# Kernel optimization log

Measured on AMD Instinct MI355X. Metric: run time of the kernel, lower is better.

## Reference

```python
import jax, jax.numpy as jnp
import numpy as np

N, E, D_IN, D_HID, D_OUT = 50000, 800000, 128, 128, 64

def setup_inputs() -> dict:
    key = jax.random.key(0)
    ks = jax.random.split(key, 20)
    inp = {
        'x': jax.random.normal(ks[0], (N, D_IN), dtype=jnp.float32),
        'edge_index': jax.random.randint(ks[1], (2, E), 0, N, dtype=jnp.int64),
        'edge_attr': jax.random.normal(ks[2], (E, 16), dtype=jnp.float32),
        'edge_weight': jax.random.uniform(ks[3], (E,), dtype=jnp.float32),
    }
    dims = [(D_IN, D_HID), (D_HID, D_HID), (D_HID, D_OUT)]
    for i, (di, do) in enumerate(dims):
        s = 1.0 / np.sqrt(di)
        inp[f'Wl{i}'] = jax.random.uniform(ks[4 + 5 * i], (di, do), minval=-s, maxval=s, dtype=jnp.float32)
        inp[f'bl{i}'] = jnp.zeros((do,), dtype=jnp.float32)
        inp[f'Wr{i}'] = jax.random.uniform(ks[5 + 5 * i], (di, do), minval=-s, maxval=s, dtype=jnp.float32)
        inp[f'Ws{i}'] = jax.random.uniform(ks[6 + 5 * i], (di, do), minval=-s, maxval=s, dtype=jnp.float32)
        inp[f'bs{i}'] = jnp.zeros((do,), dtype=jnp.float32)
    return inp


def _sage(x, src, dst, Wl, bl, Wr):
    # mean aggregation of source features at target nodes (PyG SAGEConv)
    msg = x[src]                                               # [E, d] gather
    ssum = jax.ops.segment_sum(msg, dst, num_segments=N)        # [N, d]
    cnt = jax.ops.segment_sum(jnp.ones((src.shape[0],), x.dtype), dst, num_segments=N)
    agg = ssum / jnp.maximum(cnt, 1.0)[:, None]
    return agg @ Wl + bl + x @ Wr                               # lin_l(agg) + lin_r(x)


def reference(x, edge_index, edge_attr, edge_weight,
              Wl0, bl0, Wr0, Ws0, bs0,
              Wl1, bl1, Wr1, Ws1, bs1,
              Wl2, bl2, Wr2, Ws2, bs2):
    src, dst = edge_index[0], edge_index[1]
    h = jax.nn.relu(_sage(x, src, dst, Wl0, bl0, Wr0) + x @ Ws0 + bs0)
    h = jax.nn.relu(_sage(h, src, dst, Wl1, bl1, Wr1) + h @ Ws1 + bs1)
    out = _sage(h, src, dst, Wl2, bl2, Wr2) + h @ Ws2 + bs2
    return out
```

## Files before the change

### kernel.cpp

```cpp
#include <hip/hip_runtime.h>
#include <hip/hip_bf16.h>


#define LB __launch_bounds__

typedef __attribute__((ext_vector_type(8))) short short8;
typedef __attribute__((ext_vector_type(4))) float f32x4;

__device__ __forceinline__ unsigned short bf16_rne(float f) {
  unsigned u = __builtin_bit_cast(unsigned, f);
  unsigned r = u + 0x7fffu + ((u >> 16) & 1u);
  return (unsigned short)(r >> 16);
}
__device__ __forceinline__ float bf16_to_f(unsigned short us) {
  return __builtin_bit_cast(float, (unsigned)us << 16);
}
__device__ __forceinline__ float bits_to_f(unsigned u) {
  return __builtin_bit_cast(float, u);
}

__device__ __forceinline__ void async16(const void* g, void* l) {
  __builtin_amdgcn_global_load_lds((const __attribute__((address_space(1))) unsigned*)g,
                                   (__attribute__((address_space(3))) unsigned*)l, 16, 0, 0);
}

#define BCAP 8192
#define P1_CHUNK 4096

__device__ __forceinline__ void p1_body(int bid, const int* __restrict__ src,
                                        const int* __restrict__ dst, int* __restrict__ bcnt,
                                        int2* __restrict__ pairs, int E) {
  __shared__ int cnt[256];
  __shared__ int base[256];
  const int tid = threadIdx.x;
  cnt[tid] = 0;
  __syncthreads();
  const int e0 = bid * P1_CHUNK;
  int myb[16], myr[16], mys[16], myd[16];
#pragma unroll
  for (int i = 0; i < 16; ++i) {
    int e = e0 + i * 256 + tid;
    myb[i] = -1;
    if (e < E) {
      int s = src[e], d = dst[e];
      int b = d >> 8;
      myb[i] = b;
      mys[i] = s;
      myd[i] = d;
      myr[i] = atomicAdd(&cnt[b], 1);
    }
  }
  __syncthreads();
  base[tid] = (cnt[tid] > 0) ? atomicAdd(&bcnt[tid], cnt[tid]) : 0;
  __syncthreads();
#pragma unroll
  for (int i = 0; i < 16; ++i) {
    int b = myb[i];
    if (b >= 0) {
      int p = base[b] + myr[i];
      if (p < BCAP) pairs[(size_t)b * BCAP + p] = make_int2(mys[i], myd[i]);
    }
  }
}

__device__ __forceinline__ void p234_body(int b, const int2* __restrict__ pairs,
                                          const int* __restrict__ bcnt, int* __restrict__ gcounter,
                                          int* __restrict__ row_start, int* __restrict__ deg_arr,
                                          float* __restrict__ scale, int* __restrict__ srcs, int N) {
  __shared__ int h[256];
  __shared__ int sc[256];
  __shared__ int cur[256];
  __shared__ int shared_bb;
  const int tid = threadIdx.x;
  h[tid] = 0;
  __syncthreads();
  int m = bcnt[b];
  if (m > BCAP) m = BCAP;
  for (int i = tid; i < m; i += 256) {
    atomicAdd(&h[pairs[(size_t)b * BCAP + i].y & 255], 1);
  }
  __syncthreads();
  const int deg = h[tid];
  sc[tid] = deg;
  __syncthreads();
  for (int off = 1; off < 256; off <<= 1) {
    int add = (tid >= off) ? sc[tid - off] : 0;
    __syncthreads();
    sc[tid] += add;
    __syncthreads();
  }
  if (tid == 0) shared_bb = atomicAdd(gcounter, sc[255]);
  __syncthreads();
  const int abs_off = shared_bb + sc[tid] - deg;
  const int node = b * 256 + tid;
  if (node < N) {
    row_start[node] = abs_off;
    deg_arr[node] = deg;
    scale[node] = 1.0f / (float)(deg > 1 ? deg : 1);
  }
  cur[tid] = abs_off;
  __syncthreads();
  for (int i = tid; i < m; i += 256) {
    int2 pr = pairs[(size_t)b * BCAP + i];
    int p = atomicAdd(&cur[pr.y & 255], 1);
    srcs[p] = pr.x;
  }
}

__device__ __forceinline__ void wpack_body(int wb, const float* __restrict__ Wl0,
                                           const float* __restrict__ Wr0,
                                           const float* __restrict__ Ws0,
                                           const float* __restrict__ bl0,
                                           const float* __restrict__ bs0,
                                           const float* __restrict__ Wl1,
                                           const float* __restrict__ Wr1,
                                           const float* __restrict__ Ws1,
                                           const float* __restrict__ bl1,
                                           const float* __restrict__ bs1,
                                           const float* __restrict__ Wl2,
                                           const float* __restrict__ Wr2,
                                           const float* __restrict__ Ws2,
                                           const float* __restrict__ bl2,
                                           const float* __restrict__ bs2, ushort* __restrict__ Bh0,
                                           ushort* __restrict__ Bo0, float* __restrict__ bb0,
                                           ushort* __restrict__ Bh1, ushort* __restrict__ Bo1,
                                           float* __restrict__ bb1, ushort* __restrict__ Bh2,
                                           ushort* __restrict__ Bo2, float* __restrict__ bb2) {
  const int layer = wb >> 7;
  const int xb = wb & 127;
  const float *Wl, *Wr, *Ws, *bl, *bs;
  ushort *Bh, *Bo;
  float* bb;
  int M;
  if (layer == 0) {
    Wl = Wl0; Wr = Wr0; Ws = Ws0; bl = bl0; bs = bs0; Bh = Bh0; Bo = Bo0; bb = bb0; M = 256;
  } else if (layer == 1) {
    Wl = Wl1; Wr = Wr1; Ws = Ws1; bl = bl1; bs = bs1; Bh = Bh1; Bo = Bo1; bb = bb1; M = 256;
  } else {
    Wl = Wl2; Wr = Wr2; Ws = Ws2; bl = bl2; bs = bs2; Bh = Bh2; Bo = Bo2; bb = bb2; M = 128;
  }
  const int DO = M / 2;
  int idx = xb * 256 + (int)threadIdx.x;
  if (idx < 128 * M) {
    int k = idx / M, c = idx - k * M;
    float v = (c < DO) ? Wl[k * DO + c] : (Wr[k * DO + (c - DO)] + Ws[k * DO + (c - DO)]);
    unsigned short h = bf16_rne(v);
    unsigned short l = bf16_rne(v - bf16_to_f(h));
    int d = ((k >> 3) * M + c) * 8 + (k & 7);
    Bh[d] = h;
    Bo[d] = l;
  }
  if (idx < DO) bb[idx] = bl[idx] + bs[idx];
}

__device__ __forceinline__ void split8v(f32x4 f0, f32x4 f1, short8& h, short8& l) {
  float f[8] = {f0[0], f0[1], f0[2], f0[3], f1[0], f1[1], f1[2], f1[3]};
#pragma unroll
  for (int j = 0; j < 8; ++j) {
    unsigned u = __builtin_bit_cast(unsigned, f[j]);
    h[j] = (short)(u >> 16);
    l[j] = (short)bf16_rne(f[j] - bits_to_f(u & 0xffff0000u));
  }
}

template <int M>
__device__ __forceinline__ void gemm_compute(int bx, const char* smem,
                                             const ushort* __restrict__ Bhi,
                                             const ushort* __restrict__ Blo,
                                             ushort* __restrict__ Yb, float* __restrict__ Z,
                                             int n) {
  constexpr int DO = M / 2;
  constexpr int NWC = (M >= 256) ? 4 : 2;
  constexpr int NWR = 4 / NWC;
  constexpr int BROWS = 32 * NWR;
  const int tid = threadIdx.x;
  const int w = tid >> 6, l = tid & 63;
  const int q = l >> 4, m16 = l & 15;
  const int rowBase = bx * BROWS + (w / NWC) * 32;
  const int colBase = (w % NWC) * 64;

  f32x4 acc[2][4] = {};
  const int rl0 = (w / NWC) * 32 + m16;

#pragma unroll
  for (int s = 0; s < 4; ++s) {
    short8 ah[2], al[2], bh[4], bo[4];
    const int kb = s * 4 + q;
#pragma unroll
    for (int i = 0; i < 2; ++i) {
      int rl = rl0 + i * 16;
      int g0 = (2 * kb) ^ m16;
      int g1 = (2 * kb + 1) ^ m16;
      f32x4 fa = *(const f32x4*)(smem + (size_t)rl * 512 + g0 * 16);
      f32x4 fb = *(const f32x4*)(smem + (size_t)rl * 512 + g1 * 16);
      split8v(fa, fb, ah[i], al[i]);
    }
#pragma unroll
    for (int j = 0; j < 4; ++j) {
      size_t off = ((size_t)kb * M + colBase + j * 16 + m16) * 8;
      bh[j] = *(const short8*)(Bhi + off);
      bo[j] = *(const short8*)(Blo + off);
    }
#pragma unroll
    for (int i = 0; i < 2; ++i)
#pragma unroll
      for (int j = 0; j < 4; ++j) {
        acc[i][j] = __builtin_amdgcn_mfma_f32_16x16x32_bf16(ah[i], bh[j], acc[i][j], 0, 0, 0);
        acc[i][j] = __builtin_amdgcn_mfma_f32_16x16x32_bf16(ah[i], bo[j], acc[i][j], 0, 0, 0);
        acc[i][j] = __builtin_amdgcn_mfma_f32_16x16x32_bf16(al[i], bh[j], acc[i][j], 0, 0, 0);
      }
  }

#pragma unroll
  for (int i = 0; i < 2; ++i) {
    int rb = rowBase + i * 16 + q * 4;
#pragma unroll
    for (int j = 0; j < 4; ++j) {
      int c = colBase + j * 16 + m16;
#pragma unroll
      for (int r = 0; r < 4; ++r) {
        int row = rb + r;
        if (row < n) {
          float v = acc[i][j][r];
          if (c < DO)
            Yb[(size_t)row * DO + c] = bf16_rne(v);
          else
            Z[(size_t)row * DO + (c - DO)] = v;
        }
      }
    }
  }
}

__device__ __forceinline__ void gemm0_body(int bx, const float* __restrict__ x,
                                           const ushort* __restrict__ Bh,
                                           const ushort* __restrict__ Bo, ushort* __restrict__ Yb,
                                           float* __restrict__ Z, int n, char* smem) {
  const int tid = threadIdx.x;
  const int wbase = tid & ~63;
#pragma unroll
  for (int r = 0; r < 4; ++r) {
    int ell = r * 256 + tid;
    int row = ell >> 5, gl = ell & 31;
    int grow = bx * 32 + row;
    if (grow >= n) grow = n - 1;
    int gs = gl ^ (row & 15);
    async16(x + (size_t)grow * 128 + gs * 4, smem + (size_t)(r * 256 + wbase) * 16);
  }
  __syncthreads();
  gemm_compute<256>(bx, smem, Bh, Bo, Yb, Z, n);
}

__device__ __forceinline__ void agg_gather128(const uint2* __restrict__ Yu,
                                              const int* __restrict__ srcs, int e0, int cnt,
                                              int lane, int li, int half, float& a0, float& a1,
                                              float& a2, float& a3) {
  const int end = e0 + cnt;
  const int c1 = cnt < 64 ? cnt : 64;
  int idx = (lane < c1) ? srcs[e0 + lane] : 0;
  int j = 0;
  for (; j + 16 <= c1; j += 16) {
    int s[8];
#pragma unroll
    for (int t = 0; t < 8; ++t) s[t] = __shfl(idx, j + 2 * t + half);
    uint2 u[8];
#pragma unroll
    for (int t = 0; t < 8; ++t) u[t] = Yu[(size_t)s[t] * 32 + li];
#pragma unroll
    for (int t = 0; t < 8; ++t) {
      a0 += bits_to_f(u[t].x << 16);
      a1 += bits_to_f(u[t].x & 0xffff0000u);
      a2 += bits_to_f(u[t].y << 16);
      a3 += bits_to_f(u[t].y & 0xffff0000u);
    }
  }
  if (j + 8 <= c1) {
    int s[4];
#pragma unroll
    for (int t = 0; t < 4; ++t) s[t] = __shfl(idx, j + 2 * t + half);
    uint2 u[4];
#pragma unroll
    for (int t = 0; t < 4; ++t) u[t] = Yu[(size_t)s[t] * 32 + li];
#pragma unroll
    for (int t = 0; t < 4; ++t) {
      a0 += bits_to_f(u[t].x << 16);
      a1 += bits_to_f(u[t].x & 0xffff0000u);
      a2 += bits_to_f(u[t].y << 16);
      a3 += bits_to_f(u[t].y & 0xffff0000u);
    }
    j += 8;
  }
  for (; j + 2 <= c1; j += 2) {
    int s = __shfl(idx, j + half);
    uint2 u = Yu[(size_t)s * 32 + li];
    a0 += bits_to_f(u.x << 16);
    a1 += bits_to_f(u.x & 0xffff0000u);
    a2 += bits_to_f(u.y << 16);
    a3 += bits_to_f(u.y & 0xffff0000u);
  }
  if (j < c1) {
    int s = __shfl(idx, j);
    if (half == 0) {
      uint2 u = Yu[(size_t)s * 32 + li];
      a0 += bits_to_f(u.x << 16);
      a1 += bits_to_f(u.x & 0xffff0000u);
      a2 += bits_to_f(u.y << 16);
      a3 += bits_to_f(u.y & 0xffff0000u);
    }
  }
  if (cnt > 64) {
    int e = e0 + 64;
    for (; e + 2 <= end; e += 2) {
      int s = srcs[e + half];
      uint2 u = Yu[(size_t)s * 32 + li];
      a0 += bits_to_f(u.x << 16);
      a1 += bits_to_f(u.x & 0xffff0000u);
      a2 += bits_to_f(u.y << 16);
      a3 += bits_to_f(u.y & 0xffff0000u);
    }
    if (e < end && half == 0) {
      int s = srcs[e];
      uint2 u = Yu[(size_t)s * 32 + li];
      a0 += bits_to_f(u.x << 16);
      a1 += bits_to_f(u.x & 0xffff0000u);
      a2 += bits_to_f(u.y << 16);
      a3 += bits_to_f(u.y & 0xffff0000u);
    }
  }
}

template <int M>
__global__ LB(256, 3) void fused_agg_gemm(const ushort* __restrict__ Y,
                                          const float* __restrict__ Zprev,
                                          const int* __restrict__ row_start,
                                          const int* __restrict__ deg_arr,
                                          const int* __restrict__ srcs,
                                          const float* __restrict__ scale,
                                          const float* __restrict__ bsum,
                                          const ushort* __restrict__ Bhi,
                                          const ushort* __restrict__ Blo, ushort* __restrict__ Yb,
                                          float* __restrict__ Zf, int n) {
  constexpr int BROWS = (M >= 256) ? 32 : 64;
  __shared__ __align__(16) char smem[BROWS * 512];
  const int tid = threadIdx.x;
  const int w = tid >> 6;
  const int lane = tid & 63;
  const int li = lane & 31;
  const int half = lane >> 5;
  const int blockRow0 = blockIdx.x * BROWS;
  const uint2* Yu = (const uint2*)Y;

#pragma unroll 1
  for (int t = 0; t < BROWS / 4; ++t) {
    const int r = t * 4 + w;
    const int node = blockRow0 + r;
    float a0 = 0.f, a1 = 0.f, a2 = 0.f, a3 = 0.f;
    const bool live = node < n;
    if (live) {
      agg_gather128(Yu, srcs, row_start[node], deg_arr[node], lane, li, half, a0, a1, a2, a3);
    }
    a0 += __shfl(a0, lane ^ 32);
    a1 += __shfl(a1, lane ^ 32);
    a2 += __shfl(a2, lane ^ 32);
    a3 += __shfl(a3, lane ^ 32);
    float4 o = make_float4(0.f, 0.f, 0.f, 0.f);
    if (live) {
      float sc = scale[node];
      float4 z = ((const float4*)Zprev)[(size_t)node * 32 + li];
      float4 b = ((const float4*)bsum)[li];
      o.x = fmaxf(z.x + sc * a0 + b.x, 0.f);
      o.y = fmaxf(z.y + sc * a1 + b.y, 0.f);
      o.z = fmaxf(z.z + sc * a2 + b.z, 0.f);
      o.w = fmaxf(z.w + sc * a3 + b.w, 0.f);
    }
    if (half == 0) {
      *(float4*)(smem + (size_t)r * 512 + (size_t)((li ^ (r & 15)) * 16)) = o;
    }
  }
  __syncthreads();
  gemm_compute<M>(blockIdx.x, smem, Bhi, Blo, Yb, Zf, n);
}

__global__ LB(256) void fused_wpack_p1(const int* __restrict__ src, const int* __restrict__ dst,
                                       int* __restrict__ bcnt, int2* __restrict__ pairs, int E,
                                       int NP1, const float* Wl0, const float* Wr0, const float* Ws0,
                                       const float* bl0, const float* bs0, const float* Wl1,
                                       const float* Wr1, const float* Ws1, const float* bl1,
                                       const float* bs1, const float* Wl2, const float* Wr2,
                                       const float* Ws2, const float* bl2, const float* bs2,
                                       ushort* Bh0, ushort* Bo0, float* bb0, ushort* Bh1,
                                       ushort* Bo1, float* bb1, ushort* Bh2, ushort* Bo2,
                                       float* bb2) {
  if ((int)blockIdx.x < NP1) {
    p1_body(blockIdx.x, src, dst, bcnt, pairs, E);
  } else {
    wpack_body(blockIdx.x - NP1, Wl0, Wr0, Ws0, bl0, bs0, Wl1, Wr1, Ws1, bl1, bs1, Wl2, Wr2, Ws2,
               bl2, bs2, Bh0, Bo0, bb0, Bh1, Bo1, bb1, Bh2, Bo2, bb2);
  }
}

__global__ LB(256, 3) void fused_p234_gemm0(const int2* __restrict__ pairs,
                                            const int* __restrict__ bcnt, int* __restrict__ gcounter,
                                            int* __restrict__ row_start, int* __restrict__ deg_arr,
                                            float* __restrict__ scale, int* __restrict__ srcs, int N,
                                            const float* __restrict__ x,
                                            const ushort* __restrict__ Bh0,
                                            const ushort* __restrict__ Bo0, ushort* __restrict__ Yb,
                                            float* __restrict__ Zf, int NB) {
  __shared__ __align__(16) char smem[32 * 512];
  if ((int)blockIdx.x < NB) {
    p234_body(blockIdx.x, pairs, bcnt, gcounter, row_start, deg_arr, scale, srcs, N);
  } else {
    gemm0_body(blockIdx.x - NB, x, Bh0, Bo0, Yb, Zf, N, smem);
  }
}

__global__ LB(256) void agg64_kernel(const ushort* __restrict__ Y, const float* __restrict__ Z,
                                     const int* __restrict__ row_start,
                                     const int* __restrict__ deg_arr, const int* __restrict__ srcs,
                                     const float* __restrict__ scale, const float* __restrict__ bsum,
                                     float* __restrict__ out, int n) {
  int node = blockIdx.x * 4 + (threadIdx.x >> 6);
  if (node >= n) return;
  const int lane = threadIdx.x & 63;
  const int li = lane & 15;
  const int qt = lane >> 4;
  const int e0 = row_start[node];
  const int cnt = deg_arr[node];
  const int end = e0 + cnt;
  const int c1 = cnt < 64 ? cnt : 64;
  int idx = (lane < c1) ? srcs[e0 + lane] : 0;
  const uint2* Yu = (const uint2*)Y;
  float a0 = 0.f, a1 = 0.f, a2 = 0.f, a3 = 0.f;

  int j = 0;
  for (; j + 16 <= c1; j += 16) {
    int s0 = __shfl(idx, j + qt);
    int s1 = __shfl(idx, j + 4 + qt);
    int s2 = __shfl(idx, j + 8 + qt);
    int s3 = __shfl(idx, j + 12 + qt);
    uint2 u0 = Yu[(size_t)s0 * 16 + li];
    uint2 u1 = Yu[(size_t)s1 * 16 + li];
    uint2 u2 = Yu[(size_t)s2 * 16 + li];
    uint2 u3 = Yu[(size_t)s3 * 16 + li];
    a0 += bits_to_f(u0.x << 16) + bits_to_f(u1.x << 16) + bits_to_f(u2.x << 16) +
          bits_to_f(u3.x << 16);
    a1 += bits_to_f(u0.x & 0xffff0000u) + bits_to_f(u1.x & 0xffff0000u) +
          bits_to_f(u2.x & 0xffff0000u) + bits_to_f(u3.x & 0xffff0000u);
    a2 += bits_to_f(u0.y << 16) + bits_to_f(u1.y << 16) + bits_to_f(u2.y << 16) +
          bits_to_f(u3.y << 16);
    a3 += bits_to_f(u0.y & 0xffff0000u) + bits_to_f(u1.y & 0xffff0000u) +
          bits_to_f(u2.y & 0xffff0000u) + bits_to_f(u3.y & 0xffff0000u);
  }
  for (; j + 4 <= c1; j += 4) {
    int s = __shfl(idx, j + qt);
    uint2 u = Yu[(size_t)s * 16 + li];
    a0 += bits_to_f(u.x << 16);
    a1 += bits_to_f(u.x & 0xffff0000u);
    a2 += bits_to_f(u.y << 16);
    a3 += bits_to_f(u.y & 0xffff0000u);
  }
  {
    int rem = c1 - j;
    if (rem > 0) {
      int s = __shfl(idx, j + (qt < rem ? qt : 0));
      if (qt < rem) {
        uint2 u = Yu[(size_t)s * 16 + li];
        a0 += bits_to_f(u.x << 16);
        a1 += bits_to_f(u.x & 0xffff0000u);
        a2 += bits_to_f(u.y << 16);
        a3 += bits_to_f(u.y & 0xffff0000u);
      }
    }
  }
  if (cnt > 64) {
    int e = e0 + 64;
    for (; e + 4 <= end; e += 4) {
      int s = srcs[e + qt];
      uint2 u = Yu[(size_t)s * 16 + li];
      a0 += bits_to_f(u.x << 16);
      a1 += bits_to_f(u.x & 0xffff0000u);
      a2 += bits_to_f(u.y << 16);
      a3 += bits_to_f(u.y & 0xffff0000u);
    }
    int rem = end - e;
    if (qt < rem) {
      int s = srcs[e + qt];
      uint2 u = Yu[(size_t)s * 16 + li];
      a0 += bits_to_f(u.x << 16);
      a1 += bits_to_f(u.x & 0xffff0000u);
      a2 += bits_to_f(u.y << 16);
      a3 += bits_to_f(u.y & 0xffff0000u);
    }
  }
  a0 += __shfl(a0, lane ^ 16);
  a1 += __shfl(a1, lane ^ 16);
  a2 += __shfl(a2, lane ^ 16);
  a3 += __shfl(a3, lane ^ 16);
  a0 += __shfl(a0, lane ^ 32);
  a1 += __shfl(a1, lane ^ 32);
  a2 += __shfl(a2, lane ^ 32);
  a3 += __shfl(a3, lane ^ 32);

  if (qt == 0) {
    float sc = scale[node];
    float4 z = ((const float4*)Z)[(size_t)node * 16 + li];
    float4 b = ((const float4*)bsum)[li];
    float4 o;
    o.x = z.x + sc * a0 + b.x;
    o.y = z.y + sc * a1 + b.y;
    o.z = z.z + sc * a2 + b.z;
    o.w = z.w + sc * a3 + b.w;
    ((float4*)out)[(size_t)node * 16 + li] = o;
  }
}

extern "C" void kernel_launch(void* const* d_in, const int* in_sizes, int n_in,
                              void* d_out, int out_size, void* d_ws, size_t ws_size,
                              hipStream_t stream) {
  const float* x = (const float*)d_in[0];
  const int* ei = (const int*)d_in[1];
  const int N = in_sizes[0] / 128;
  const int E = in_sizes[3];
  const int* src = ei;
  const int* dst = ei + E;
  const float* Wl[3] = {(const float*)d_in[4], (const float*)d_in[9], (const float*)d_in[14]};
  const float* bl[3] = {(const float*)d_in[5], (const float*)d_in[10], (const float*)d_in[15]};
  const float* Wr[3] = {(const float*)d_in[6], (const float*)d_in[11], (const float*)d_in[16]};
  const float* Ws[3] = {(const float*)d_in[7], (const float*)d_in[12], (const float*)d_in[17]};
  const float* bs[3] = {(const float*)d_in[8], (const float*)d_in[13], (const float*)d_in[18]};

  const int NB = (N + 255) >> 8;
  const int NP1 = (E + P1_CHUNK - 1) / P1_CHUNK;

  size_t off = 0;
  auto carve = [&](size_t bytes) -> char* {
    char* p = (char*)d_ws + off;
    off += (bytes + 255) & ~(size_t)255;
    return p;
  };
  int* row_start = (int*)carve((size_t)N * 4);
  int* deg_arr = (int*)carve((size_t)N * 4);
  int* bcnt = (int*)carve((size_t)NB * 4);
  int* gcounter = (int*)carve(256);
  float* scale = (float*)carve((size_t)N * 4);
  int* srcs = (int*)carve((size_t)E * 4);
  int2* pairs = (int2*)carve((size_t)NB * BCAP * 8);
  ushort* Yb0 = (ushort*)carve((size_t)N * 128 * 2);
  float* Zf0 = (float*)carve((size_t)N * 128 * 4);
  ushort* Yb1 = (ushort*)carve((size_t)N * 128 * 2);
  float* Zf1 = (float*)carve((size_t)N * 128 * 4);
  ushort* Bh[3];
  ushort* Bo[3];
  float* bsum[3];
  for (int i = 0; i < 3; ++i) {
    Bh[i] = (ushort*)carve(128 * 256 * 2);
    Bo[i] = (ushort*)carve(128 * 256 * 2);
    bsum[i] = (float*)carve(128 * 4);
  }
  (void)ws_size;
  (void)n_in;
  (void)out_size;

  size_t bcnt_pad = ((size_t)NB * 4 + 255) & ~(size_t)255;
  hipMemsetAsync(bcnt, 0, bcnt_pad + 4, stream);

  fused_wpack_p1<<<NP1 + 384, 256, 0, stream>>>(
      src, dst, bcnt, pairs, E, NP1, Wl[0], Wr[0], Ws[0], bl[0], bs[0], Wl[1], Wr[1], Ws[1], bl[1],
      bs[1], Wl[2], Wr[2], Ws[2], bl[2], bs[2], Bh[0], Bo[0], bsum[0], Bh[1], Bo[1], bsum[1], Bh[2],
      Bo[2], bsum[2]);

  int g32 = (N + 31) / 32;
  int g64 = (N + 63) / 64;
  int gAgg = (N + 3) / 4;

  fused_p234_gemm0<<<NB + g32, 256, 0, stream>>>(pairs, bcnt, gcounter, row_start, deg_arr, scale,
                                                 srcs, N, x, Bh[0], Bo[0], Yb0, Zf0, NB);
  fused_agg_gemm<256><<<g32, 256, 0, stream>>>(Yb0, Zf0, row_start, deg_arr, srcs, scale, bsum[0],
                                               Bh[1], Bo[1], Yb1, Zf1, N);
  fused_agg_gemm<128><<<g64, 256, 0, stream>>>(Yb1, Zf1, row_start, deg_arr, srcs, scale, bsum[1],
                                               Bh[2], Bo[2], Yb0, Zf0, N);
  agg64_kernel<<<gAgg, 256, 0, stream>>>(Yb0, Zf0, row_start, deg_arr, srcs, scale, bsum[2],
                                         (float*)d_out, N);
}
```

Baseline: 306.7 us.

## Stage block edge indices in LDS and gather 16-byte rows per quarter-wave

Each block now preloads its contiguous CSR edge source indices and row starts and degrees into shared memory, instead of reading them per node from global memory with shuffles. The gather is restructured so that four 16-lane groups each fetch a full 256-byte bf16 row with uint4 loads, giving four edges in flight per wave step instead of two. A butterfly shuffle reduces the partial sums. This trades extra LDS (up to 16KB of indices), which may cut occupancy, and adds a global fallback path for blocks whose edges overflow the staging buffer.

```diff
diff --git a/kernel.cpp b/kernel.cpp
--- a/kernel.cpp
+++ b/kernel.cpp
@@ -251,82 +251,15 @@
   gemm_compute<256>(bx, smem, Bh, Bo, Yb, Z, n);
 }
 
-__device__ __forceinline__ void agg_gather128(const uint2* __restrict__ Yu,
-                                              const int* __restrict__ srcs, int e0, int cnt,
-                                              int lane, int li, int half, float& a0, float& a1,
-                                              float& a2, float& a3) {
-  const int end = e0 + cnt;
-  const int c1 = cnt < 64 ? cnt : 64;
-  int idx = (lane < c1) ? srcs[e0 + lane] : 0;
-  int j = 0;
-  for (; j + 16 <= c1; j += 16) {
-    int s[8];
-#pragma unroll
-    for (int t = 0; t < 8; ++t) s[t] = __shfl(idx, j + 2 * t + half);
-    uint2 u[8];
-#pragma unroll
-    for (int t = 0; t < 8; ++t) u[t] = Yu[(size_t)s[t] * 32 + li];
-#pragma unroll
-    for (int t = 0; t < 8; ++t) {
-      a0 += bits_to_f(u[t].x << 16);
-      a1 += bits_to_f(u[t].x & 0xffff0000u);
-      a2 += bits_to_f(u[t].y << 16);
-      a3 += bits_to_f(u[t].y & 0xffff0000u);
-    }
-  }
-  if (j + 8 <= c1) {
-    int s[4];
-#pragma unroll
-    for (int t = 0; t < 4; ++t) s[t] = __shfl(idx, j + 2 * t + half);
-    uint2 u[4];
-#pragma unroll
-    for (int t = 0; t < 4; ++t) u[t] = Yu[(size_t)s[t] * 32 + li];
-#pragma unroll
-    for (int t = 0; t < 4; ++t) {
-      a0 += bits_to_f(u[t].x << 16);
-      a1 += bits_to_f(u[t].x & 0xffff0000u);
-      a2 += bits_to_f(u[t].y << 16);
-      a3 += bits_to_f(u[t].y & 0xffff0000u);
-    }
-    j += 8;
-  }
-  for (; j + 2 <= c1; j += 2) {
-    int s = __shfl(idx, j + half);
-    uint2 u = Yu[(size_t)s * 32 + li];
-    a0 += bits_to_f(u.x << 16);
-    a1 += bits_to_f(u.x & 0xffff0000u);
-    a2 += bits_to_f(u.y << 16);
-    a3 += bits_to_f(u.y & 0xffff0000u);
-  }
-  if (j < c1) {
-    int s = __shfl(idx, j);
-    if (half == 0) {
-      uint2 u = Yu[(size_t)s * 32 + li];
-      a0 += bits_to_f(u.x << 16);
-      a1 += bits_to_f(u.x & 0xffff0000u);
-      a2 += bits_to_f(u.y << 16);
-      a3 += bits_to_f(u.y & 0xffff0000u);
-    }
-  }
-  if (cnt > 64) {
-    int e = e0 + 64;
-    for (; e + 2 <= end; e += 2) {
-      int s = srcs[e + half];
-      uint2 u = Yu[(size_t)s * 32 + li];
-      a0 += bits_to_f(u.x << 16);
-      a1 += bits_to_f(u.x & 0xffff0000u);
-      a2 += bits_to_f(u.y << 16);
-      a3 += bits_to_f(u.y & 0xffff0000u);
-    }
-    if (e < end && half == 0) {
-      int s = srcs[e];
-      uint2 u = Yu[(size_t)s * 32 + li];
-      a0 += bits_to_f(u.x << 16);
-      a1 += bits_to_f(u.x & 0xffff0000u);
-      a2 += bits_to_f(u.y << 16);
-      a3 += bits_to_f(u.y & 0xffff0000u);
-    }
-  }
+__device__ __forceinline__ void acc8(float* a, uint4 u) {
+  a[0] += bits_to_f(u.x << 16);
+  a[1] += bits_to_f(u.x & 0xffff0000u);
+  a[2] += bits_to_f(u.y << 16);
+  a[3] += bits_to_f(u.y & 0xffff0000u);
+  a[4] += bits_to_f(u.z << 16);
+  a[5] += bits_to_f(u.z & 0xffff0000u);
+  a[6] += bits_to_f(u.w << 16);
+  a[7] += bits_to_f(u.w & 0xffff0000u);
 }
 
 template <int M>
@@ -341,40 +274,122 @@
                                           const ushort* __restrict__ Blo, ushort* __restrict__ Yb,
                                           float* __restrict__ Zf, int n) {
   constexpr int BROWS = (M >= 256) ? 32 : 64;
+  constexpr int ECAP = (M >= 256) ? 2048 : 4096;
   __shared__ __align__(16) char smem[BROWS * 512];
+  __shared__ int eidx[ECAP];
+  __shared__ int rs_s[BROWS];
+  __shared__ int deg_s[BROWS];
   const int tid = threadIdx.x;
   const int w = tid >> 6;
   const int lane = tid & 63;
-  const int li = lane & 31;
-  const int half = lane >> 5;
+  const int qt = lane >> 4;
+  const int li = lane & 15;
   const int blockRow0 = blockIdx.x * BROWS;
-  const uint2* Yu = (const uint2*)Y;
-
-#pragma unroll 1
+  const uint4* Y4 = (const uint4*)Y;
+
+  if (tid < BROWS) {
+    int node = blockRow0 + tid;
+    int cn = node < n ? node : n - 1;
+    rs_s[tid] = row_start[cn];
+    deg_s[tid] = node < n ? deg_arr[node] : 0;
+  }
+  __syncthreads();
+  const int lastValid = (n - blockRow0 < BROWS ? n - blockRow0 : BROWS) - 1;
+  const int rs0 = rs_s[0];
+  const int total = rs_s[lastValid] + deg_s[lastValid] - rs0;
+  const int stage = total < ECAP ? total : ECAP;
+  for (int i = tid; i < stage; i += 256) eidx[i] = srcs[rs0 + i];
+  __syncthreads();
+
+#pragma unroll 2
   for (int t = 0; t < BROWS / 4; ++t) {
     const int r = t * 4 + w;
     const int node = blockRow0 + r;
-    float a0 = 0.f, a1 = 0.f, a2 = 0.f, a3 = 0.f;
     const bool live = node < n;
+    float a[8] = {0.f, 0.f, 0.f, 0.f, 0.f, 0.f, 0.f, 0.f};
+    float4 z0, z1, b0, b1;
+    float sc = 0.f;
     if (live) {
-      agg_gather128(Yu, srcs, row_start[node], deg_arr[node], lane, li, half, a0, a1, a2, a3);
-    }
-    a0 += __shfl(a0, lane ^ 32);
-    a1 += __shfl(a1, lane ^ 32);
-    a2 += __shfl(a2, lane ^ 32);
-    a3 += __shfl(a3, lane ^ 32);
-    float4 o = make_float4(0.f, 0.f, 0.f, 0.f);
-    if (live) {
-      float sc = scale[node];
-      float4 z = ((const float4*)Zprev)[(size_t)node * 32 + li];
-      float4 b = ((const float4*)bsum)[li];
-      o.x = fmaxf(z.x + sc * a0 + b.x, 0.f);
-      o.y = fmaxf(z.y + sc * a1 + b.y, 0.f);
-      o.z = fmaxf(z.z + sc * a2 + b.z, 0.f);
-      o.w = fmaxf(z.w + sc * a3 + b.w, 0.f);
-    }
-    if (half == 0) {
-      *(float4*)(smem + (size_t)r * 512 + (size_t)((li ^ (r & 15)) * 16)) = o;
+      const int base = rs_s[r] - rs0;
+      const int cnt = deg_s[r];
+      if (qt == 0) {
+        sc = scale[node];
+        z0 = ((const float4*)Zprev)[(size_t)node * 32 + 2 * li];
+        z1 = ((const float4*)Zprev)[(size_t)node * 32 + 2 * li + 1];
+        b0 = ((const float4*)bsum)[2 * li];
+        b1 = ((const float4*)bsum)[2 * li + 1];
+      }
+      int avail = ECAP - base;
+      if (avail < 0) avail = 0;
+      const int cin = cnt < avail ? cnt : avail;
+      int j = 0;
+      for (; j + 16 <= cin; j += 16) {
+        int s0 = eidx[base + j + qt];
+        int s1 = eidx[base + j + 4 + qt];
+        int s2 = eidx[base + j + 8 + qt];
+        int s3 = eidx[base + j + 12 + qt];
+        uint4 u0 = Y4[(size_t)s0 * 16 + li];
+        uint4 u1 = Y4[(size_t)s1 * 16 + li];
+        uint4 u2 = Y4[(size_t)s2 * 16 + li];
+        uint4 u3 = Y4[(size_t)s3 * 16 + li];
+        acc8(a, u0);
+        acc8(a, u1);
+        acc8(a, u2);
+        acc8(a, u3);
+      }
+      for (; j + 4 <= cin; j += 4) {
+        int s = eidx[base + j + qt];
+        uint4 u = Y4[(size_t)s * 16 + li];
+        acc8(a, u);
+      }
+      {
+        int rem = cin - j;
+        if (rem > 0) {
+          int s = eidx[base + j + (qt < rem ? qt : 0)];
+          if (qt < rem) {
+            uint4 u = Y4[(size_t)s * 16 + li];
+            acc8(a, u);
+          }
+        }
+      }
+      if (cin < cnt) {
+        int e = cin;
+        const int abs0 = rs_s[r];
+        for (; e + 4 <= cnt; e += 4) {
+          int s = srcs[abs0 + e + qt];
+          uint4 u = Y4[(size_t)s * 16 + li];
+          acc8(a, u);
+        }
+        int rem = cnt - e;
+        if (rem > 0) {
+          int s = srcs[abs0 + e + (qt < rem ? qt : 0)];
+          if (qt < rem) {
+            uint4 u = Y4[(size_t)s * 16 + li];
+            acc8(a, u);
+          }
+        }
+      }
+    }
+#pragma unroll
+    for (int k = 0; k < 8; ++k) {
+      a[k] += __shfl(a[k], lane ^ 16);
+      a[k] += __shfl(a[k], lane ^ 32);
+    }
+    float4 o0 = make_float4(0.f, 0.f, 0.f, 0.f);
+    float4 o1 = make_float4(0.f, 0.f, 0.f, 0.f);
+    if (live && qt == 0) {
+      o0.x = fmaxf(z0.x + sc * a[0] + b0.x, 0.f);
+      o0.y = fmaxf(z0.y + sc * a[1] + b0.y, 0.f);
+      o0.z = fmaxf(z0.z + sc * a[2] + b0.z, 0.f);
+      o0.w = fmaxf(z0.w + sc * a[3] + b0.w, 0.f);
+      o1.x = fmaxf(z1.x + sc * a[4] + b1.x, 0.f);
+      o1.y = fmaxf(z1.y + sc * a[5] + b1.y, 0.f);
+      o1.z = fmaxf(z1.z + sc * a[6] + b1.z, 0.f);
+      o1.w = fmaxf(z1.w + sc * a[7] + b1.w, 0.f);
+    }
+    if (qt == 0) {
+      *(float4*)(smem + (size_t)r * 512 + (size_t)(((2 * li) ^ (r & 15)) * 16)) = o0;
+      *(float4*)(smem + (size_t)r * 512 + (size_t)(((2 * li + 1) ^ (r & 15)) * 16)) = o1;
     }
   }
   __syncthreads();
```

Result: slower. 315.1 us (+2.7%).
